# Kernel tuning notes

Hardware: AMD Instinct MI355X
Metric: run time of the kernel (lower is better)

## Reference

```python
import jax, jax.numpy as jnp
import numpy as np

N_NODES = 50000
N_EDGES = 800000
D = 64


def setup_inputs() -> dict:
    key = jax.random.key(0)
    k = jax.random.split(key, 8)
    h = jax.random.normal(k[0], (N_NODES, D), dtype=jnp.float32)
    edge_src = jax.random.randint(k[1], (N_EDGES,), 0, N_NODES, dtype=jnp.int32)
    edge_dst = jax.random.randint(k[2], (N_EDGES,), 0, N_NODES, dtype=jnp.int32)
    # normalized adjacency weights (e.g. 1/deg style values in (0,1))
    edge_w = jax.random.uniform(k[3], (N_EDGES,), dtype=jnp.float32)
    W_self = jax.random.normal(k[4], (D, D), dtype=jnp.float32) / np.sqrt(D)
    b_self = jnp.zeros((D,), dtype=jnp.float32)
    W_neigh = jax.random.normal(k[5], (D, D), dtype=jnp.float32) / np.sqrt(D)
    b_neigh = jnp.zeros((D,), dtype=jnp.float32)
    return {
        "h": h,
        "edge_src": edge_src,
        "edge_dst": edge_dst,
        "edge_w": edge_w,
        "W_self": W_self,
        "b_self": b_self,
        "W_neigh": W_neigh,
        "b_neigh": b_neigh,
    }


def reference(h, edge_src, edge_dst, edge_w, W_self, b_self, W_neigh, b_neigh):
    # neigh = A_norm @ h : sparse COO matmul as weighted gather + segment-sum
    # messages: [E, D]
    msgs = edge_w[:, None] * h[edge_src]
    neigh = jax.ops.segment_sum(msgs, edge_dst, num_segments=N_NODES)  # [N, D]
    # out = lin_self(h) + lin_neigh(neigh), relu; dropout is a no-op in eval mode
    out = (h @ W_self.T + b_self) + (neigh @ W_neigh.T + b_neigh)
    return jax.nn.relu(out)
```

## Files before the change

### kernel.cpp

```cpp
#include <hip/hip_runtime.h>

#define N_NODES 50000
#define N_EDGES 800000
#define D 64

#define NPB 200
#define NB  250
#define CAP 4096
#define BT  512
#define EPT 4
#define CHUNK_E (BT * EPT)
#define NCHUNKS ((N_EDGES + CHUNK_E - 1) / CHUNK_E)
#define CT  1024
#define GBLK 16

typedef unsigned short ushort_t;
typedef unsigned int   uint_t;
typedef __attribute__((ext_vector_type(8))) short   short8;
typedef __attribute__((ext_vector_type(4))) float   float4v;

__device__ __forceinline__ ushort_t f2b(float f) {
    uint_t u = __float_as_uint(f);
    return (ushort_t)((u + 0x7FFFu + ((u >> 16) & 1u)) >> 16);
}
__device__ __forceinline__ float b2f(ushort_t b) {
    return __uint_as_float((uint_t)b << 16);
}
__device__ __forceinline__ uint_t rne_hi16(uint_t u) {
    return (u + 0x7FFFu + ((u >> 16) & 1u)) & 0xFFFF0000u;
}
__device__ __forceinline__ float lane_bcast(float v, int l) {
    return __int_as_float(__builtin_amdgcn_readlane(__float_as_int(v), l));
}


__global__ __launch_bounds__(BT) void bin_h2b_kernel(
    const int* __restrict__ src, const int* __restrict__ dst,
    const float* __restrict__ w, int* __restrict__ cursor,
    int2* __restrict__ bedges,
    const float* __restrict__ h, ushort_t* __restrict__ hb)
{
    if (blockIdx.x >= NCHUNKS) {
        const int nb = gridDim.x - NCHUNKS;
        for (int i = (blockIdx.x - NCHUNKS) * BT + threadIdx.x;
             i < N_NODES * D / 4; i += nb * BT) {
            const float4 v = ((const float4*)h)[i];
            ushort4 o;
            o.x = f2b(v.x); o.y = f2b(v.y); o.z = f2b(v.z); o.w = f2b(v.w);
            ((ushort4*)hb)[i] = o;
        }
        return;
    }

    __shared__ int lh[NB];
    __shared__ int loff[NB];
    __shared__ int lcur[NB];
    __shared__ int gpos[NB];
    __shared__ int part[256];
    __shared__ int2 stage[CHUNK_E];
    __shared__ unsigned char sbk[CHUNK_E];

    const int t = threadIdx.x;
    for (int i = t; i < NB; i += BT) lh[i] = 0;
    __syncthreads();

    const int base = blockIdx.x * CHUNK_E;
    int   my_b[EPT];
    int   my_p[EPT];
    float my_w[EPT];
#pragma unroll
    for (int k = 0; k < EPT; ++k) {
        const int e = base + k * BT + t;
        if (e < N_EDGES) {
            const int d = dst[e];
            const int b = (unsigned)d / NPB;
            my_b[k] = b;
            my_p[k] = (src[e] << 8) | (d - b * NPB);
            my_w[k] = w[e];
            atomicAdd(&lh[b], 1);
        } else {
            my_b[k] = -1;
        }
    }
    __syncthreads();

    const int v = (t < NB) ? lh[t] : 0;
    if (t < 256) part[t] = v;
    __syncthreads();
    for (int off = 1; off < 256; off <<= 1) {
        int p = 0;
        if (t < 256 && t >= off) p = part[t - off];
        __syncthreads();
        if (t < 256) part[t] += p;
        __syncthreads();
    }
    if (t < NB) { loff[t] = part[t] - v; lcur[t] = part[t] - v; }
    __syncthreads();

#pragma unroll
    for (int k = 0; k < EPT; ++k) {
        if (my_b[k] >= 0) {
            const int p = atomicAdd(&lcur[my_b[k]], 1);
            stage[p] = make_int2(my_p[k], __float_as_int(my_w[k]));
            sbk[p] = (unsigned char)my_b[k];
        }
    }
    __syncthreads();

    if (t < NB && lh[t] > 0)
        gpos[t] = t * CAP + atomicAdd(&cursor[t], lh[t]);
    __syncthreads();

    const int tot = min(N_EDGES - base, CHUNK_E);
    for (int s = t; s < tot; s += BT) {
        const int b = sbk[s];
        bedges[gpos[b] + (s - loff[b])] = stage[s];
    }
}

__global__ __launch_bounds__(CT) void bucket_csr_kernel(
    const int* __restrict__ cursor, const int2* __restrict__ bedges,
    uint_t* __restrict__ pedges, int2* __restrict__ offs2)
{
    __shared__ int    lcur[NPB];
    __shared__ int    part[256];
    __shared__ uint_t stage[CAP];

    const int b   = blockIdx.x;
    const int t   = threadIdx.x;
    const int gb  = b * CAP;
    const int cnt = min(cursor[b], CAP);

    if (t < NPB) lcur[t] = 0;
    __syncthreads();
    for (int e = t; e < cnt; e += CT)
        atomicAdd(&lcur[bedges[gb + e].x & 255], 1);
    __syncthreads();

    const int v = (t < NPB) ? lcur[t] : 0;
    if (t < 256) part[t] = v;
    __syncthreads();
    for (int off = 1; off < 256; off <<= 1) {
        int p = 0;
        if (t < 256 && t >= off) p = part[t - off];
        __syncthreads();
        if (t < 256) part[t] += p;
        __syncthreads();
    }
    if (t < NPB) {
        const int ex = part[t] - v;
        lcur[t] = ex;
        offs2[b * NPB + t] = make_int2(gb + ex, gb + ex + v);
    }
    __syncthreads();

    for (int e = t; e < cnt; e += CT) {
        const int2 r = bedges[gb + e];
        const int p = atomicAdd(&lcur[r.x & 255], 1);
        stage[p] = (uint_t)(r.x >> 8) | rne_hi16((uint_t)r.y);
    }
    __syncthreads();
    for (int s = t; s < cnt; s += CT)
        pedges[gb + s] = stage[s];
}

__global__ __launch_bounds__(512) void gather_linear_kernel(
    const ushort_t* __restrict__ hb, const uint_t* __restrict__ pedges,
    const int2* __restrict__ offs2,
    const float* __restrict__ Ws, const float* __restrict__ bs,
    const float* __restrict__ Wn, const float* __restrict__ bn,
    float* __restrict__ out)
{
    __shared__ ushort_t nstage[GBLK * D];

    const int wave  = threadIdx.x >> 6;
    const int lane  = threadIdx.x & 63;
    const int node0 = blockIdx.x * GBLK;

#pragma unroll
    for (int jj = 0; jj < 2; ++jj) {
        const int j = wave * 2 + jj;
        const int node = node0 + j;
        if (node < N_NODES) {
            const int2 be = offs2[node];
            const int beg = be.x, end = be.y;
            float acc = 0.f;
            int e = beg;
            for (; e + 16 <= end; e += 16) {
                uint_t r[16];
                float  vv[16];
#pragma unroll
                for (int k = 0; k < 16; ++k) r[k] = pedges[e + k];
#pragma unroll
                for (int k = 0; k < 16; ++k)
                    vv[k] = b2f(hb[(size_t)(r[k] & 0xFFFFu) * D + lane]);
#pragma unroll
                for (int k = 0; k < 16; ++k)
                    acc = fmaf(__uint_as_float(r[k] & 0xFFFF0000u), vv[k], acc);
            }
            for (; e + 4 <= end; e += 4) {
                uint_t r[4];
                float  vv[4];
#pragma unroll
                for (int k = 0; k < 4; ++k) r[k] = pedges[e + k];
#pragma unroll
                for (int k = 0; k < 4; ++k)
                    vv[k] = b2f(hb[(size_t)(r[k] & 0xFFFFu) * D + lane]);
#pragma unroll
                for (int k = 0; k < 4; ++k)
                    acc = fmaf(__uint_as_float(r[k] & 0xFFFF0000u), vv[k], acc);
            }
            for (; e < end; ++e) {
                const uint_t r = pedges[e];
                acc = fmaf(__uint_as_float(r & 0xFFFF0000u),
                           b2f(hb[(size_t)(r & 0xFFFFu) * D + lane]), acc);
            }
            nstage[j * D + lane] = f2b(acc);
        }
    }
    __syncthreads();

    const int nt = wave;
    if (nt >= 4 || node0 >= N_NODES) return;
    const int row16 = lane & 15;
    const int quad  = lane >> 4;

    const size_t abase = (size_t)(node0 + row16) * D + quad * 8;
    const short8 ah0 = *(const short8*)(hb + abase);
    const short8 ah1 = *(const short8*)(hb + abase + 32);
    const ushort_t* sp = nstage + row16 * D + quad * 8;
    const short8 an0 = *(const short8*)sp;
    const short8 an1 = *(const short8*)(sp + 32);

    const int col = nt * 16 + row16;
    const float* wsr = Ws + (size_t)col * D + quad * 8;
    const float* wnr = Wn + (size_t)col * D + quad * 8;
    short8 bw[4];
#pragma unroll
    for (int f = 0; f < 4; ++f) {
        const float* p = (f < 2 ? wsr : wnr) + (f & 1) * 32;
        const float4 w0 = *(const float4*)p;
        const float4 w1 = *(const float4*)(p + 4);
        short8 bwv;
        bwv[0] = (short)f2b(w0.x); bwv[1] = (short)f2b(w0.y);
        bwv[2] = (short)f2b(w0.z); bwv[3] = (short)f2b(w0.w);
        bwv[4] = (short)f2b(w1.x); bwv[5] = (short)f2b(w1.y);
        bwv[6] = (short)f2b(w1.z); bwv[7] = (short)f2b(w1.w);
        bw[f] = bwv;
    }
    float4v acc = {0.f, 0.f, 0.f, 0.f};
    acc = __builtin_amdgcn_mfma_f32_16x16x32_bf16(ah0, bw[0], acc, 0, 0, 0);
    acc = __builtin_amdgcn_mfma_f32_16x16x32_bf16(ah1, bw[1], acc, 0, 0, 0);
    acc = __builtin_amdgcn_mfma_f32_16x16x32_bf16(an0, bw[2], acc, 0, 0, 0);
    acc = __builtin_amdgcn_mfma_f32_16x16x32_bf16(an1, bw[3], acc, 0, 0, 0);

    const float bias = bs[col] + bn[col];
#pragma unroll
    for (int r = 0; r < 4; ++r) {
        const int m = quad * 4 + r;
        out[(size_t)(node0 + m) * D + col] = fmaxf(acc[r] + bias, 0.f);
    }
}

__global__ __launch_bounds__(256) void sage_scatter(
    const float* __restrict__ h,
    const int* __restrict__ edge_src,
    const int* __restrict__ edge_dst,
    const float* __restrict__ edge_w,
    float* __restrict__ neigh)
{
    const long long tid = (long long)blockIdx.x * blockDim.x + threadIdx.x;
    const int e = (int)(tid >> 6);
    const int d = (int)(tid & 63);
    if (e >= N_EDGES) return;
    atomicAdd(&neigh[(long long)edge_dst[e] * D + d],
              edge_w[e] * h[(long long)edge_src[e] * D + d]);
}

__global__ __launch_bounds__(256, 2) void linear_f32_kernel(
    const float* __restrict__ h, const float* __restrict__ neigh,
    const float* __restrict__ Ws, const float* __restrict__ bs,
    const float* __restrict__ Wn, const float* __restrict__ bn,
    float* __restrict__ out)
{
    const int lane   = threadIdx.x & 63;
    const int gwave  = (blockIdx.x * blockDim.x + threadIdx.x) >> 6;
    const int nwaves = (gridDim.x * blockDim.x) >> 6;

    float Wsr[D], Wnr[D];
#pragma unroll
    for (int k = 0; k < D; k += 4) {
        const float4 a = *(const float4*)&Ws[(size_t)lane * D + k];
        const float4 b = *(const float4*)&Wn[(size_t)lane * D + k];
        Wsr[k] = a.x; Wsr[k+1] = a.y; Wsr[k+2] = a.z; Wsr[k+3] = a.w;
        Wnr[k] = b.x; Wnr[k+1] = b.y; Wnr[k+2] = b.z; Wnr[k+3] = b.w;
    }
    const float bias = bs[lane] + bn[lane];

    for (int n = gwave; n < N_NODES; n += nwaves) {
        const float hv = h[(size_t)n * D + lane];
        const float nv = neigh[(size_t)n * D + lane];
        float o = bias;
#pragma unroll
        for (int k = 0; k < D; ++k) {
            o = fmaf(lane_bcast(hv, k), Wsr[k], o);
            o = fmaf(lane_bcast(nv, k), Wnr[k], o);
        }
        out[(size_t)n * D + lane] = fmaxf(o, 0.f);
    }
}

extern "C" void kernel_launch(void* const* d_in, const int* in_sizes, int n_in,
                              void* d_out, int out_size, void* d_ws, size_t ws_size,
                              hipStream_t stream)
{
    const float* h        = (const float*)d_in[0];
    const int*   edge_src = (const int*)d_in[1];
    const int*   edge_dst = (const int*)d_in[2];
    const float* edge_w   = (const float*)d_in[3];
    const float* W_self   = (const float*)d_in[4];
    const float* b_self   = (const float*)d_in[5];
    const float* W_neigh  = (const float*)d_in[6];
    const float* b_neigh  = (const float*)d_in[7];
    float*       out      = (float*)d_out;

    int2*     bedges = (int2*)d_ws;
    uint_t*   pedges = (uint_t*)(bedges + (size_t)NB * CAP);
    int2*     offs2  = (int2*)(pedges + (size_t)NB * CAP);
    ushort_t* hb     = (ushort_t*)(offs2 + N_NODES);
    int*      cursor = (int*)(hb + (size_t)N_NODES * D);
    const size_t needed = (size_t)NB * CAP * 8 + (size_t)NB * CAP * 4
                        + (size_t)N_NODES * 8 + (size_t)N_NODES * D * 2 + NB * 4;

    if (ws_size >= needed) {
        hipMemsetAsync(cursor, 0, NB * sizeof(int), stream);
        bin_h2b_kernel<<<NCHUNKS * 2, BT, 0, stream>>>(
            edge_src, edge_dst, edge_w, cursor, bedges, h, hb);
        bucket_csr_kernel<<<NB, CT, 0, stream>>>(cursor, bedges, pedges, offs2);
        gather_linear_kernel<<<(N_NODES + GBLK - 1) / GBLK, 512, 0, stream>>>(
            hb, pedges, offs2, W_self, b_self, W_neigh, b_neigh, out);
    } else {
        float* neigh_fb = (float*)d_ws;
        hipMemsetAsync(neigh_fb, 0, (size_t)N_NODES * D * sizeof(float), stream);
        const long long total = (long long)N_EDGES * 64;
        sage_scatter<<<(int)((total + 255) / 256), 256, 0, stream>>>(
            h, edge_src, edge_dst, edge_w, neigh_fb);
        linear_f32_kernel<<<1024, 256, 0, stream>>>(h, neigh_fb, W_self, b_self,
                                                    W_neigh, b_neigh, out);
    }
}
```

Baseline: 145.3 us.

## Replace two-pass bucket sort with global histogram, scan, and atomic scatter CSR build

Replaces the block-local bucket binning plus per-bucket counting sort with a three-step CSR build. It takes a global per-node histogram of destinations, does a per-bucket prefix scan into node offsets, and then scatters packed src/weight records with global atomics on per-node cursors. This drops the intermediate 8-byte bedges buffer and one full read/write pass, and uses vectorized int4 loads. In exchange it relies on many contended global atomics (two per edge) and gives up deterministic edge order within a node.

```diff
diff --git a/kernel.cpp b/kernel.cpp
--- a/kernel.cpp
+++ b/kernel.cpp
@@ -7,12 +7,15 @@
 #define NPB 200
 #define NB  250
 #define CAP 4096
-#define BT  512
-#define EPT 4
-#define CHUNK_E (BT * EPT)
-#define NCHUNKS ((N_EDGES + CHUNK_E - 1) / CHUNK_E)
-#define CT  1024
 #define GBLK 16
+
+#define HT 512
+#define HEPT 4
+#define HBLK ((N_EDGES + HT * HEPT - 1) / (HT * HEPT))
+
+#define ST 256
+#define SEPT 4
+#define SBLK ((N_EDGES + ST * SEPT - 1) / (ST * SEPT))
 
 typedef unsigned short ushort_t;
 typedef unsigned int   uint_t;
@@ -34,16 +37,14 @@
 }
 
 
-__global__ __launch_bounds__(BT) void bin_h2b_kernel(
-    const int* __restrict__ src, const int* __restrict__ dst,
-    const float* __restrict__ w, int* __restrict__ cursor,
-    int2* __restrict__ bedges,
+__global__ __launch_bounds__(HT) void hist_h2b_kernel(
+    const int* __restrict__ dst, int* __restrict__ cnt,
     const float* __restrict__ h, ushort_t* __restrict__ hb)
 {
-    if (blockIdx.x >= NCHUNKS) {
-        const int nb = gridDim.x - NCHUNKS;
-        for (int i = (blockIdx.x - NCHUNKS) * BT + threadIdx.x;
-             i < N_NODES * D / 4; i += nb * BT) {
+    if (blockIdx.x >= HBLK) {
+        const int nb = gridDim.x - HBLK;
+        for (int i = (blockIdx.x - HBLK) * HT + threadIdx.x;
+             i < N_NODES * D / 4; i += nb * HT) {
             const float4 v = ((const float4*)h)[i];
             ushort4 o;
             o.x = f2b(v.x); o.y = f2b(v.y); o.z = f2b(v.z); o.w = f2b(v.w);
@@ -52,116 +53,83 @@
         return;
     }
 
-    __shared__ int lh[NB];
-    __shared__ int loff[NB];
-    __shared__ int lcur[NB];
-    __shared__ int gpos[NB];
+    const int e0 = (blockIdx.x * HT + threadIdx.x) * HEPT;
+    if (e0 + HEPT <= N_EDGES) {
+        const int4 d4 = *(const int4*)(dst + e0);
+        atomicAdd(&cnt[d4.x], 1);
+        atomicAdd(&cnt[d4.y], 1);
+        atomicAdd(&cnt[d4.z], 1);
+        atomicAdd(&cnt[d4.w], 1);
+    } else {
+        for (int e = e0; e < N_EDGES; ++e) atomicAdd(&cnt[dst[e]], 1);
+    }
+}
+
+__global__ __launch_bounds__(256) void bucket_scan_kernel(
+    const int* __restrict__ cnt, int2* __restrict__ offs2,
+    int* __restrict__ ncur)
+{
     __shared__ int part[256];
-    __shared__ int2 stage[CHUNK_E];
-    __shared__ unsigned char sbk[CHUNK_E];
-
+    const int b = blockIdx.x;
     const int t = threadIdx.x;
-    for (int i = t; i < NB; i += BT) lh[i] = 0;
-    __syncthreads();
-
-    const int base = blockIdx.x * CHUNK_E;
-    int   my_b[EPT];
-    int   my_p[EPT];
-    float my_w[EPT];
-#pragma unroll
-    for (int k = 0; k < EPT; ++k) {
-        const int e = base + k * BT + t;
-        if (e < N_EDGES) {
-            const int d = dst[e];
-            const int b = (unsigned)d / NPB;
-            my_b[k] = b;
-            my_p[k] = (src[e] << 8) | (d - b * NPB);
-            my_w[k] = w[e];
-            atomicAdd(&lh[b], 1);
-        } else {
-            my_b[k] = -1;
-        }
-    }
-    __syncthreads();
-
-    const int v = (t < NB) ? lh[t] : 0;
-    if (t < 256) part[t] = v;
+    const int gb = b * CAP;
+
+    const int v = (t < NPB) ? cnt[b * NPB + t] : 0;
+    part[t] = v;
     __syncthreads();
     for (int off = 1; off < 256; off <<= 1) {
         int p = 0;
-        if (t < 256 && t >= off) p = part[t - off];
+        if (t >= off) p = part[t - off];
         __syncthreads();
-        if (t < 256) part[t] += p;
+        part[t] += p;
         __syncthreads();
     }
-    if (t < NB) { loff[t] = part[t] - v; lcur[t] = part[t] - v; }
-    __syncthreads();
-
-#pragma unroll
-    for (int k = 0; k < EPT; ++k) {
-        if (my_b[k] >= 0) {
-            const int p = atomicAdd(&lcur[my_b[k]], 1);
-            stage[p] = make_int2(my_p[k], __float_as_int(my_w[k]));
-            sbk[p] = (unsigned char)my_b[k];
-        }
-    }
-    __syncthreads();
-
-    if (t < NB && lh[t] > 0)
-        gpos[t] = t * CAP + atomicAdd(&cursor[t], lh[t]);
-    __syncthreads();
-
-    const int tot = min(N_EDGES - base, CHUNK_E);
-    for (int s = t; s < tot; s += BT) {
-        const int b = sbk[s];
-        bedges[gpos[b] + (s - loff[b])] = stage[s];
-    }
-}
-
-__global__ __launch_bounds__(CT) void bucket_csr_kernel(
-    const int* __restrict__ cursor, const int2* __restrict__ bedges,
-    uint_t* __restrict__ pedges, int2* __restrict__ offs2)
-{
-    __shared__ int    lcur[NPB];
-    __shared__ int    part[256];
-    __shared__ uint_t stage[CAP];
-
-    const int b   = blockIdx.x;
-    const int t   = threadIdx.x;
-    const int gb  = b * CAP;
-    const int cnt = min(cursor[b], CAP);
-
-    if (t < NPB) lcur[t] = 0;
-    __syncthreads();
-    for (int e = t; e < cnt; e += CT)
-        atomicAdd(&lcur[bedges[gb + e].x & 255], 1);
-    __syncthreads();
-
-    const int v = (t < NPB) ? lcur[t] : 0;
-    if (t < 256) part[t] = v;
-    __syncthreads();
-    for (int off = 1; off < 256; off <<= 1) {
-        int p = 0;
-        if (t < 256 && t >= off) p = part[t - off];
-        __syncthreads();
-        if (t < 256) part[t] += p;
-        __syncthreads();
-    }
     if (t < NPB) {
-        const int ex = part[t] - v;
-        lcur[t] = ex;
-        offs2[b * NPB + t] = make_int2(gb + ex, gb + ex + v);
-    }
-    __syncthreads();
-
-    for (int e = t; e < cnt; e += CT) {
-        const int2 r = bedges[gb + e];
-        const int p = atomicAdd(&lcur[r.x & 255], 1);
-        stage[p] = (uint_t)(r.x >> 8) | rne_hi16((uint_t)r.y);
-    }
-    __syncthreads();
-    for (int s = t; s < cnt; s += CT)
-        pedges[gb + s] = stage[s];
+        const int ex  = part[t] - v;
+        const int beg = gb + min(ex, CAP);
+        const int end = gb + min(ex + v, CAP);
+        offs2[b * NPB + t] = make_int2(beg, end);
+        ncur[b * NPB + t]  = beg;
+    }
+}
+
+__global__ __launch_bounds__(ST) void scatter_kernel(
+    const int* __restrict__ src, const int* __restrict__ dst,
+    const float* __restrict__ w, int* __restrict__ ncur,
+    uint_t* __restrict__ pedges)
+{
+    const int e0 = (blockIdx.x * ST + threadIdx.x) * SEPT;
+    if (e0 >= N_EDGES) return;
+
+    if (e0 + SEPT <= N_EDGES) {
+        const int4   s4 = *(const int4*)(src + e0);
+        const int4   d4 = *(const int4*)(dst + e0);
+        const float4 w4 = *(const float4*)(w + e0);
+        const int   s[4]  = { s4.x, s4.y, s4.z, s4.w };
+        const int   d[4]  = { d4.x, d4.y, d4.z, d4.w };
+        const float ww[4] = { w4.x, w4.y, w4.z, w4.w };
+        uint_t rec[4];
+        int    p[4];
+#pragma unroll
+        for (int k = 0; k < SEPT; ++k)
+            rec[k] = (uint_t)s[k] | rne_hi16(__float_as_uint(ww[k]));
+#pragma unroll
+        for (int k = 0; k < SEPT; ++k)
+            p[k] = atomicAdd(&ncur[d[k]], 1);
+#pragma unroll
+        for (int k = 0; k < SEPT; ++k) {
+            const int bend = (int)((unsigned)d[k] / NPB) * CAP + CAP;
+            if (p[k] < bend) pedges[p[k]] = rec[k];
+        }
+    } else {
+        for (int e = e0; e < N_EDGES; ++e) {
+            const int dd = dst[e];
+            const uint_t rec = (uint_t)src[e] | rne_hi16(__float_as_uint(w[e]));
+            const int p = atomicAdd(&ncur[dd], 1);
+            const int bend = (int)((unsigned)dd / NPB) * CAP + CAP;
+            if (p < bend) pedges[p] = rec;
+        }
+    }
 }
 
 __global__ __launch_bounds__(512) void gather_linear_kernel(
@@ -324,19 +292,21 @@
     const float* b_neigh  = (const float*)d_in[7];
     float*       out      = (float*)d_out;
 
-    int2*     bedges = (int2*)d_ws;
-    uint_t*   pedges = (uint_t*)(bedges + (size_t)NB * CAP);
+    uint_t*   pedges = (uint_t*)d_ws;
     int2*     offs2  = (int2*)(pedges + (size_t)NB * CAP);
     ushort_t* hb     = (ushort_t*)(offs2 + N_NODES);
-    int*      cursor = (int*)(hb + (size_t)N_NODES * D);
-    const size_t needed = (size_t)NB * CAP * 8 + (size_t)NB * CAP * 4
-                        + (size_t)N_NODES * 8 + (size_t)N_NODES * D * 2 + NB * 4;
+    int*      cnt    = (int*)(hb + (size_t)N_NODES * D);
+    int*      ncur   = cnt + N_NODES;
+    const size_t needed = (size_t)NB * CAP * 4 + (size_t)N_NODES * 8
+                        + (size_t)N_NODES * D * 2
+                        + (size_t)N_NODES * 4 + (size_t)N_NODES * 4;
 
     if (ws_size >= needed) {
-        hipMemsetAsync(cursor, 0, NB * sizeof(int), stream);
-        bin_h2b_kernel<<<NCHUNKS * 2, BT, 0, stream>>>(
-            edge_src, edge_dst, edge_w, cursor, bedges, h, hb);
-        bucket_csr_kernel<<<NB, CT, 0, stream>>>(cursor, bedges, pedges, offs2);
+        hipMemsetAsync(cnt, 0, N_NODES * sizeof(int), stream);
+        hist_h2b_kernel<<<HBLK * 2, HT, 0, stream>>>(edge_dst, cnt, h, hb);
+        bucket_scan_kernel<<<NB, 256, 0, stream>>>(cnt, offs2, ncur);
+        scatter_kernel<<<SBLK, ST, 0, stream>>>(edge_src, edge_dst, edge_w,
+                                                ncur, pedges);
         gather_linear_kernel<<<(N_NODES + GBLK - 1) / GBLK, 512, 0, stream>>>(
             hb, pedges, offs2, W_self, b_self, W_neigh, b_neigh, out);
     } else {
```

After: 207.9 us. +43.1%, slower.
